# Optimization experiments

Hardware: AMD Instinct MI355X
Metric: run time of the kernel (lower is better)

## Reference

```python
import jax, jax.numpy as jnp
import numpy as np

B, C, H, W = 4, 64, 160, 160
OUT = 64
KS = (5, 7)


def conv2d(x, w, b=None, pad=0, groups=1):
    y = jax.lax.conv_general_dilated(
        x, w, (1, 1), [(pad, pad), (pad, pad)],
        feature_group_count=groups,
        dimension_numbers=('NCHW', 'OIHW', 'NCHW'))
    return y if b is None else y + b[None, :, None, None]


def bn_eval(x, g, b, m, v, eps=1e-5):
    s = g / jnp.sqrt(v + eps)
    return x * s[None, :, None, None] + (b - m * s)[None, :, None, None]


def boundary_attn(x, w1, b1, w2, b2):
    Cc = x.shape[1]
    kx = jnp.array([[-1., 0., 1.], [-2., 0., 2.], [-1., 0., 1.]], jnp.float32)
    ky = jnp.array([[-1., -2., -1.], [0., 0., 0.], [1., 2., 1.]], jnp.float32)
    sobel = jnp.concatenate([jnp.tile(kx[None, None], (Cc, 1, 1, 1)),
                             jnp.tile(ky[None, None], (Cc, 1, 1, 1))], axis=0)  # [2C,1,3,3]
    # grouped conv (groups=C): same output-channel grouping semantics as torch
    edge = jnp.abs(conv2d(x, sobel, pad=1, groups=Cc))
    edge = (edge[:, :Cc] + edge[:, Cc:]).mean(axis=1, keepdims=True)
    a = jax.nn.relu(conv2d(x, w1, b1, pad=1))
    a = conv2d(a, w2, b2, pad=0)
    a = jax.nn.sigmoid(a + edge)
    return x * a + x


def icc(off, half_k):
    # iterative cumulative constraint over the (small, static) K channel axis
    K = off.shape[1]
    cs = [None] * K
    cs[half_k] = off[:, half_k]
    for i in range(1, half_k + 1):
        cs[half_k - i] = 0.5 * cs[half_k - i + 1] + 0.5 * off[:, half_k - i]
        cs[half_k + i] = 0.5 * cs[half_k + i - 1] + 0.5 * off[:, half_k + i]
    c = jnp.stack(cs, axis=1)
    w = jnp.ones((K, 1, 3, 3), jnp.float32) / 9.0
    return conv2d(c, w, pad=1, groups=K)


def tumor_center(x):
    _, _, Hx, Wx = x.shape
    fs = x.mean(axis=1)  # [B,H,W]
    hg = jnp.arange(Hx, dtype=x.dtype)[None, :, None]
    wg = jnp.arange(Wx, dtype=x.dtype)[None, None, :]
    tot = fs.sum(axis=(1, 2)) + 1e-6
    return (fs * hg).sum(axis=(1, 2)) / tot, (fs * wg).sum(axis=(1, 2)) / tot


def dyn1d(x, kw, kb, K, O):
    # Original Dynamic1DConv reshapes x to [B*H*W, C, 1, 1] and grid_samples a
    # [1,K] grid per pixel. With align_corners=True a 1x1 input maps every grid
    # coordinate to ix=iy=0, so sampled[n,c,k] == x[b,c,h,w] for all k; the
    # bmm with per-pixel kernels followed by sum over C therefore collapses to
    # (sum_c x) * (sum_k kernels) -- same math, no giant gather materialized.
    Bx, _, Hx, Wx = x.shape
    ker = conv2d(x, kw, kb, pad=0).reshape(Bx, O, K, Hx, Wx)
    return x.sum(axis=1, keepdims=True) * ker.sum(axis=2)


def reference(x, ba_w1, ba_b1, ba_w2, ba_b2,
              off_w1, off_b1, off_bn_g, off_bn_b, off_bn_m, off_bn_v,
              off_w2, off_b2,
              rk5_w, rk5_b, rk7_w, rk7_b,
              lk5_w, lk5_b, lk7_w, lk7_b,
              sf_w, sf_b, sf_bn_g, sf_bn_b, sf_bn_m, sf_bn_v,
              fc_w, fc_b):
    residual = x  # in_channels == out_channels -> nn.Identity
    xa = boundary_attn(x, ba_w1, ba_b1, ba_w2, ba_b2)
    # offset branch (faithful to original; mathematically dead because the
    # per-pixel grid_sample ignores its grid -- see dyn1d). BN in eval mode.
    raw = conv2d(xa, off_w1, off_b1, pad=1)
    raw = jax.nn.relu(bn_eval(raw, off_bn_g, off_bn_b, off_bn_m, off_bn_v))
    raw = conv2d(raw, off_w2, off_b2, pad=1)
    sumk, idx = sum(KS), 0
    _offs = []
    for k in KS:
        _offs.append(icc(jnp.tanh(raw[:, idx:idx + k]), k // 2))
        _offs.append(icc(jnp.tanh(raw[:, sumk + idx:sumk + idx + k]), k // 2))
        idx += k
    _hc, _wc = tumor_center(xa)  # also dead w.r.t. output
    O = OUT // 2 // len(KS)  # 16 channels per scale per flow type
    feats = [dyn1d(xa, rk5_w, rk5_b, 5, O), dyn1d(xa, rk7_w, rk7_b, 7, O),
             dyn1d(xa, lk5_w, lk5_b, 5, O), dyn1d(xa, lk7_w, lk7_b, 7, O)]
    fusion = jnp.concatenate(feats, axis=1)  # [B, OUT, H, W]
    y = jax.nn.relu(bn_eval(conv2d(fusion, sf_w, sf_b, pad=1),
                            sf_bn_g, sf_bn_b, sf_bn_m, sf_bn_v))
    y = conv2d(y, fc_w, fc_b, pad=0)
    return y + residual


def setup_inputs() -> dict:
    key = jax.random.key(0)
    keys = iter(jax.random.split(key, 40))
    def nrm(shape, s=0.05):
        return jax.random.normal(next(keys), shape, jnp.float32) * s
    d = {}
    d['x'] = nrm((B, C, H, W), 1.0)
    d['ba_w1'] = nrm((C // 2, C, 3, 3)); d['ba_b1'] = nrm((C // 2,))
    d['ba_w2'] = nrm((1, C // 2, 1, 1)); d['ba_b2'] = nrm((1,))
    d['off_w1'] = nrm((C // 2, C, 3, 3)); d['off_b1'] = nrm((C // 2,))
    d['off_bn_g'] = 1.0 + nrm((C // 2,)); d['off_bn_b'] = nrm((C // 2,))
    d['off_bn_m'] = nrm((C // 2,))
    d['off_bn_v'] = jax.random.uniform(next(keys), (C // 2,), jnp.float32, 0.5, 1.5)
    d['off_w2'] = nrm((2 * sum(KS), C // 2, 3, 3)); d['off_b2'] = nrm((2 * sum(KS),))
    O = OUT // 2 // len(KS)
    for name, k in (('rk5', 5), ('rk7', 7), ('lk5', 5), ('lk7', 7)):
        d[name + '_w'] = nrm((O * k, C, 1, 1)); d[name + '_b'] = nrm((O * k,))
    d['sf_w'] = nrm((OUT, OUT, 3, 3)); d['sf_b'] = nrm((OUT,))
    d['sf_bn_g'] = 1.0 + nrm((OUT,)); d['sf_bn_b'] = nrm((OUT,))
    d['sf_bn_m'] = nrm((OUT,))
    d['sf_bn_v'] = jax.random.uniform(next(keys), (OUT,), jnp.float32, 0.5, 1.5)
    d['fc_w'] = nrm((OUT, OUT, 1, 1)); d['fc_b'] = nrm((OUT,))
    return d
```

## Files before the change

### kernel.cpp

```cpp
#include <hip/hip_runtime.h>
#include <hip/hip_bf16.h>
#include <math.h>

#define BB 4
#define CC 64
#define HH 160
#define WW 160
#define HWs (HH*WW)
#define NPIX (BB*HWs)

using bf16 = __hip_bfloat16;
typedef __attribute__((ext_vector_type(8)))  short short8v;
typedef __attribute__((ext_vector_type(16))) float float16v;

__device__ __forceinline__ unsigned short f2bfu(float f){
    union { bf16 h; unsigned short u; } cv; cv.h = __float2bfloat16(f); return cv.u;
}
__device__ __forceinline__ float bfu2f(unsigned short u){
    union { float f; unsigned int i; } cv; cv.i = ((unsigned int)u)<<16; return cv.f;
}
__device__ __forceinline__ float16v fzero16(){
    float16v z;
    #pragma unroll
    for(int i=0;i<16;i++) z[i]=0.f;
    return z;
}

constexpr int B1X1 = 0;
constexpr int SFBo = 64;
constexpr int SFWf = 128;
constexpr int BAWf = 18560;
constexpr int FUWf = 27776;
constexpr int FCWf = 29824;
constexpr int WS_FLOATS = 31872;

__global__ void k_prep(const float* __restrict__ rk5w, const float* __restrict__ rk5b,
                       const float* __restrict__ rk7w, const float* __restrict__ rk7b,
                       const float* __restrict__ lk5w, const float* __restrict__ lk5b,
                       const float* __restrict__ lk7w, const float* __restrict__ lk7b,
                       const float* __restrict__ sfw,  const float* __restrict__ sfb,
                       const float* __restrict__ bng,  const float* __restrict__ bnb,
                       const float* __restrict__ bnm,  const float* __restrict__ bnv,
                       const float* __restrict__ baw1, const float* __restrict__ fcw,
                       float* __restrict__ ws)
{
    int tid = blockIdx.x*blockDim.x + threadIdx.x;
    int nt  = gridDim.x*blockDim.x;
    for(int o=tid;o<64;o+=nt){
        int grp=o>>4, oo=o&15; int K=(grp&1)?7:5;
        const float* bp = (grp==0)?rk5b:(grp==1)?rk7b:(grp==2)?lk5b:lk7b;
        float s=0.f; for(int k=0;k<K;k++) s += bp[oo*K+k];
        ws[B1X1+o]=s;
    }
    for(int oc=tid;oc<64;oc+=nt){
        float sc = bng[oc]*rsqrtf(bnv[oc]+1e-5f);
        ws[SFBo+oc] = sfb[oc]*sc + bnb[oc] - bnm[oc]*sc;
    }
    unsigned short* sfwf = (unsigned short*)(ws + SFWf);
    for(int idx=tid; idx<36864; idx+=nt){
        int og = idx/18432;  int rem = idx - og*18432;
        int f  = rem>>9;     int r2 = rem & 511;
        int lane = r2>>3;    int j = r2&7;
        int tap = f>>2, kc = f&3;
        int oc = og*32 + (lane&31);
        int ic = kc*16 + (lane>>5)*8 + j;
        float sc = bng[oc]*rsqrtf(bnv[oc]+1e-5f);
        sfwf[idx] = f2bfu(sfw[(oc*64+ic)*9 + tap] * sc);
    }
    unsigned short* bawf = (unsigned short*)(ws + BAWf);
    for(int idx=tid; idx<18432; idx+=nt){
        int f  = idx>>9;     int r2 = idx & 511;
        int lane = r2>>3;    int j = r2&7;
        int tap = f>>2, kc = f&3;
        int oc = lane&31;
        int ic = kc*16 + (lane>>5)*8 + j;
        bawf[idx] = f2bfu(baw1[(oc*64+ic)*9 + tap]);
    }
    unsigned short* fuwf = (unsigned short*)(ws + FUWf);
    for(int idx=tid; idx<4096; idx+=nt){
        int og   = idx>>11;
        int kc   = (idx>>9)&3;
        int lane = (idx>>3)&63;
        int j    = idx&7;
        int oc = og*32 + (lane&31);
        int c  = kc*16 + (lane>>5)*8 + j;
        int grp = oc>>4, oo = oc&15; int K = (grp&1)?7:5;
        const float* w = (grp==0)?rk5w:(grp==1)?rk7w:(grp==2)?lk5w:lk7w;
        float s = 0.f;
        for(int k=0;k<K;k++) s += w[(oo*K+k)*64 + c];
        fuwf[idx] = f2bfu(s);
    }
    unsigned short* fcwf = (unsigned short*)(ws + FCWf);
    for(int idx=tid; idx<4096; idx+=nt){
        int og   = idx>>11;
        int kc   = (idx>>9)&3;
        int lane = (idx>>3)&63;
        int j    = idx&7;
        int oc = og*32 + (lane&31);
        int c  = kc*16 + (lane>>5)*8 + j;
        fcwf[idx] = f2bfu(fcw[oc*64 + c]);
    }
}

__global__ __launch_bounds__(256)
void k_x2nhwc(const float* __restrict__ x, unsigned short* __restrict__ xb)
{
    __shared__ unsigned short ls[128*72];
    const int t = threadIdx.x;
    const int p0 = blockIdx.x*128;
    const int b = p0 / HWs, pp0 = p0 % HWs;
    const float* xbase = x + (size_t)b*CC*HWs + pp0;
    #pragma unroll
    for(int iter=0; iter<32; iter++){
        int idx = iter*256 + t;
        int c = idx>>7, px = idx&127;
        int bs = (c>>3) ^ ((px>>3)&7);
        ls[px*72 + bs*8 + (c&7)] = f2bfu(xbase[(size_t)c*HWs + px]);
    }
    __syncthreads();
    #pragma unroll
    for(int iter=0; iter<4; iter++){
        int idx = iter*256 + t;
        int sub = idx&7, px = idx>>3;
        int bs = sub ^ ((px>>3)&7);
        short8v v = *(short8v*)(ls + px*72 + bs*8);
        *(short8v*)(xb + ((size_t)(p0+px))*64 + sub*8) = v;
    }
}

__global__ __launch_bounds__(256)
void k_fuseA(const unsigned short* __restrict__ xb, const float* __restrict__ bab1,
             const float* __restrict__ baw2, const float* __restrict__ bab2,
             const float* __restrict__ ws, unsigned short* __restrict__ fus)
{
    __shared__ unsigned short tile[10*18*72];
    __shared__ float zbuf[8][16];
    __shared__ float ebuf[2][128];
    __shared__ float sxbuf[8][16];
    __shared__ float pbuf[128], qbuf[128];
    const int bw = blockIdx.x, bh = blockIdx.y, b = blockIdx.z;
    const int t = threadIdx.x;
    const int wave = t>>6, lane = t&63;
    const int half = lane>>5, n = lane&31;
    const int w0 = bw*16, h0 = bh*8;

    const unsigned short* fb = xb + (size_t)b*HWs*64;
    for(int idx=t; idx<1440; idx+=256){
        int sub = idx&7; int pix = idx>>3;
        int row = pix/18, col = pix%18;
        int gh = h0-1+row, gw = w0-1+col;
        short8v v = {0,0,0,0,0,0,0,0};
        if(gh>=0&&gh<HH&&gw>=0&&gw<WW)
            v = *(const short8v*)(fb + ((size_t)(gh*WW+gw))*64 + sub*8);
        *(short8v*)(tile + (row*18+col)*72 + sub*8) = v;
    }
    float b1v[16], w2v[16];
    #pragma unroll
    for(int r=0;r<16;r++){
        int oc = (r&3) + 8*(r>>2) + 4*half;
        b1v[r] = bab1[oc];
        w2v[r] = baw2[oc];
    }
    __syncthreads();

    const unsigned short* bawf = (const unsigned short*)(ws + BAWf);
    {
        const int rbase = 2*wave + (n>>4);
        const int cbase = n&15;
        float16v acc = fzero16();
        #pragma unroll
        for(int kc=0; kc<4; kc++){
            short8v af[9];
            #pragma unroll
            for(int tap=0; tap<9; tap++)
                af[tap] = *(const short8v*)(bawf + (((size_t)(tap*4+kc))*64 + lane)*8);
            #pragma unroll
            for(int tap=0; tap<9; tap++){
                const int dh = tap/3, dw = tap%3;
                short8v bf = *(const short8v*)(tile + ((rbase+dh)*18 + cbase+dw)*72
                                               + kc*16 + half*8);
                acc = __builtin_amdgcn_mfma_f32_32x32x16_bf16(af[tap], bf, acc, 0,0,0);
            }
        }
        float cz = 0.f;
        #pragma unroll
        for(int r=0;r<16;r++) cz += fmaxf(acc[r]+b1v[r],0.f)*w2v[r];
        cz += __shfl_xor(cz, 32);
        if(lane < 32) zbuf[2*wave + (n>>4)][n&15] = cz;
    }
    {
        short8v ones;
        #pragma unroll
        for(int j=0;j<8;j++) ones[j] = (short)0x3F80;
        float16v s = fzero16();
        const int rr = 2*wave + (n>>4) + 1, cc = (n&15) + 1;
        #pragma unroll
        for(int kc=0; kc<4; kc++){
            short8v bf = *(const short8v*)(tile + (rr*18 + cc)*72 + kc*16 + half*8);
            s = __builtin_amdgcn_mfma_f32_32x32x16_bf16(ones, bf, s, 0,0,0);
        }
        if(lane < 32) sxbuf[2*wave + (n>>4)][n&15] = s[0];
    }
    {
        const int hf = t>>7, px = t&127;
        const int r = px>>4, c = px&15;
        float e = 0.f;
        #pragma unroll
        for(int s=0; s<4; s++){
            const int sub = hf*4 + s;
            if(hf==0){
                short8v a0 = *(const short8v*)(tile + ((r  )*18 + c  )*72 + sub*8);
                short8v a2 = *(const short8v*)(tile + ((r  )*18 + c+2)*72 + sub*8);
                short8v a3 = *(const short8v*)(tile + ((r+1)*18 + c  )*72 + sub*8);
                short8v a5 = *(const short8v*)(tile + ((r+1)*18 + c+2)*72 + sub*8);
                short8v a6 = *(const short8v*)(tile + ((r+2)*18 + c  )*72 + sub*8);
                short8v a8 = *(const short8v*)(tile + ((r+2)*18 + c+2)*72 + sub*8);
                #pragma unroll
                for(int j=0;j<8;j++){
                    float gx = (bfu2f((unsigned short)a2[j]) - bfu2f((unsigned short)a0[j]))
                       + 2.f*(bfu2f((unsigned short)a5[j]) - bfu2f((unsigned short)a3[j]))
                       +      (bfu2f((unsigned short)a8[j]) - bfu2f((unsigned short)a6[j]));
                    e += fabsf(gx);
                }
            } else {
                short8v b0 = *(const short8v*)(tile + ((r  )*18 + c  )*72 + sub*8);
                short8v b1 = *(const short8v*)(tile + ((r  )*18 + c+1)*72 + sub*8);
                short8v b2 = *(const short8v*)(tile + ((r  )*18 + c+2)*72 + sub*8);
                short8v b6 = *(const short8v*)(tile + ((r+2)*18 + c  )*72 + sub*8);
                short8v b7 = *(const short8v*)(tile + ((r+2)*18 + c+1)*72 + sub*8);
                short8v b8 = *(const short8v*)(tile + ((r+2)*18 + c+2)*72 + sub*8);
                #pragma unroll
                for(int j=0;j<8;j++){
                    float gy = (bfu2f((unsigned short)b6[j]) - bfu2f((unsigned short)b0[j]))
                       + 2.f*(bfu2f((unsigned short)b7[j]) - bfu2f((unsigned short)b1[j]))
                       +      (bfu2f((unsigned short)b8[j]) - bfu2f((unsigned short)b2[j]));
                    e += fabsf(gy);
                }
            }
        }
        ebuf[hf][px] = e;
    }
    __syncthreads();

    if(t < 128){
        const int row = t>>4, col = t&15;
        float z = zbuf[row][col] + bab2[0]
                + (ebuf[0][t] + ebuf[1][t]) * (1.f/32.f);
        float A = 1.f + 1.f/(1.f+__expf(-z));
        float S = A * sxbuf[row][col];
        pbuf[t] = A*S;
        qbuf[t] = S;
    }
    __syncthreads();

    {
        const int og = wave&1;
        const unsigned short* fuwf = (const unsigned short*)(ws + FUWf);
        short8v wf[4];
        #pragma unroll
        for(int kc=0; kc<4; kc++)
            wf[kc] = *(const short8v*)(fuwf + (((size_t)og*4 + kc)*64 + lane)*8);
        float bqv[16];
        #pragma unroll
        for(int r=0;r<16;r++) bqv[r] = ws[B1X1 + og*32 + (r&3)+8*(r>>2)+4*half];
        #pragma unroll
        for(int t2=0; t2<2; t2++){
            const int rp = (wave>>1) + 2*t2;
            const int row = 2*rp + (n>>4), col = n&15;
            float16v a = fzero16();
            #pragma unroll
            for(int kc=0; kc<4; kc++){
                short8v bf = *(const short8v*)(tile + ((row+1)*18 + col+1)*72
                                               + kc*16 + half*8);
                a = __builtin_amdgcn_mfma_f32_32x32x16_bf16(wf[kc], bf, a, 0,0,0);
            }
            const float P = pbuf[row*16+col], Q = qbuf[row*16+col];
            unsigned short* base = fus + ((size_t)b*HWs + (h0+row)*WW + w0+col)*64
                                   + og*32 + 4*half;
            #pragma unroll
            for(int g=0; g<4; g++){
                union { unsigned long long u; unsigned short s[4]; } pk;
                #pragma unroll
                for(int rr=0; rr<4; rr++)
                    pk.s[rr] = f2bfu(P*a[4*g+rr] + Q*bqv[4*g+rr]);
                *(unsigned long long*)(base + 8*g) = pk.u;
            }
        }
    }
}

__global__ __launch_bounds__(256)
void k_fuseB(const unsigned short* __restrict__ fus, const float* __restrict__ ws,
             const float* __restrict__ fcb, const float* __restrict__ x,
             float* __restrict__ out)
{
    __shared__ unsigned short ftile[10*18*72];
    __shared__ unsigned short ytile[128*72];
    const int bw = blockIdx.x, bh = blockIdx.y, b = blockIdx.z;
    const int t  = threadIdx.x;
    const int wave = t>>6, lane = t&63;
    const int half = lane>>5, n = lane&31;
    const int og = wave&1;
    const int w0 = bw*16, h0 = bh*8;

    const unsigned short* fb = fus + (size_t)b*HWs*64;
    for(int idx=t; idx<1440; idx+=256){
        int sub = idx&7; int pix = idx>>3;
        int row = pix/18, col = pix%18;
        int gh = h0-1+row, gw = w0-1+col;
        short8v v = {0,0,0,0,0,0,0,0};
        if(gh>=0&&gh<HH&&gw>=0&&gw<WW)
            v = *(const short8v*)(fb + ((size_t)(gh*WW+gw))*64 + sub*8);
        *(short8v*)(ftile + (row*18+col)*72 + sub*8) = v;
    }
    float biasv[16];
    #pragma unroll
    for(int r=0;r<16;r++) biasv[r] = ws[SFBo + og*32 + (r&3)+8*(r>>2)+4*half];
    __syncthreads();

    const unsigned short* sfwf = (const unsigned short*)(ws + SFWf);
    const int rp0 = wave>>1, rp1 = rp0+2;
    const int row0 = 2*rp0 + (n>>4), row1 = 2*rp1 + (n>>4), col = n&15;
    {
        float16v A0 = fzero16(), A1 = fzero16();
        #pragma unroll
        for(int kc=0; kc<4; kc++){
            short8v af[9];
            #pragma unroll
            for(int tap=0; tap<9; tap++)
                af[tap] = *(const short8v*)(sfwf + (((size_t)og*36 + tap*4+kc)*64 + lane)*8);
            #pragma unroll
            for(int tap=0; tap<9; tap++){
                const int dh = tap/3, dw = tap%3;
                short8v b0 = *(const short8v*)(ftile + ((row0+dh)*18 + col+dw)*72
                                               + kc*16 + half*8);
                short8v b1 = *(const short8v*)(ftile + ((row1+dh)*18 + col+dw)*72
                                               + kc*16 + half*8);
                A0 = __builtin_amdgcn_mfma_f32_32x32x16_bf16(af[tap], b0, A0, 0,0,0);
                A1 = __builtin_amdgcn_mfma_f32_32x32x16_bf16(af[tap], b1, A1, 0,0,0);
            }
        }
        unsigned short* y0 = ytile + (row0*16+col)*72 + og*32 + 4*half;
        unsigned short* y1p = ytile + (row1*16+col)*72 + og*32 + 4*half;
        #pragma unroll
        for(int g=0; g<4; g++){
            union { unsigned long long u; unsigned short s[4]; } pk0, pk1;
            #pragma unroll
            for(int rr=0; rr<4; rr++){
                pk0.s[rr] = f2bfu(fmaxf(A0[4*g+rr] + biasv[4*g+rr], 0.f));
                pk1.s[rr] = f2bfu(fmaxf(A1[4*g+rr] + biasv[4*g+rr], 0.f));
            }
            *(unsigned long long*)(y0  + 8*g) = pk0.u;
            *(unsigned long long*)(y1p + 8*g) = pk1.u;
        }
    }
    __syncthreads();

    {
        const unsigned short* fcwf = (const unsigned short*)(ws + FCWf);
        short8v ff[4];
        #pragma unroll
        for(int kc=0; kc<4; kc++)
            ff[kc] = *(const short8v*)(fcwf + (((size_t)og*4 + kc)*64 + lane)*8);
        float fcbv[16];
        #pragma unroll
        for(int r=0;r<16;r++) fcbv[r] = fcb[og*32 + (r&3)+8*(r>>2)+4*half];
        #pragma unroll
        for(int t2=0; t2<2; t2++){
            const int rp = (wave>>1) + 2*t2;
            const int row = 2*rp + (n>>4);
            const int px = row*16 + col;
            float16v F = fzero16();
            #pragma unroll
            for(int kc=0; kc<4; kc++){
                short8v bf = *(const short8v*)(ytile + px*72 + kc*16 + half*8);
                F = __builtin_amdgcn_mfma_f32_32x32x16_bf16(ff[kc], bf, F, 0,0,0);
            }
            #pragma unroll
            for(int r=0;r<16;r++){
                int oc = og*32 + (r&3)+8*(r>>2)+4*half;
                size_t g = ((size_t)(b*CC + oc))*HWs + (h0+row)*WW + w0 + col;
                out[g] = F[r] + fcbv[r] + x[g];
            }
        }
    }
}

extern "C" void kernel_launch(void* const* d_in, const int* in_sizes, int n_in,
                              void* d_out, int out_size, void* d_ws, size_t ws_size,
                              hipStream_t stream)
{
    const float* x     = (const float*)d_in[0];
    const float* ba_w1 = (const float*)d_in[1];
    const float* ba_b1 = (const float*)d_in[2];
    const float* ba_w2 = (const float*)d_in[3];
    const float* ba_b2 = (const float*)d_in[4];
    const float* rk5_w = (const float*)d_in[13];
    const float* rk5_b = (const float*)d_in[14];
    const float* rk7_w = (const float*)d_in[15];
    const float* rk7_b = (const float*)d_in[16];
    const float* lk5_w = (const float*)d_in[17];
    const float* lk5_b = (const float*)d_in[18];
    const float* lk7_w = (const float*)d_in[19];
    const float* lk7_b = (const float*)d_in[20];
    const float* sf_w  = (const float*)d_in[21];
    const float* sf_b  = (const float*)d_in[22];
    const float* bng   = (const float*)d_in[23];
    const float* bnb   = (const float*)d_in[24];
    const float* bnm   = (const float*)d_in[25];
    const float* bnv   = (const float*)d_in[26];
    const float* fc_w  = (const float*)d_in[27];
    const float* fc_b  = (const float*)d_in[28];

    float* wsf = (float*)d_ws;
    unsigned short* XB  = (unsigned short*)((char*)d_ws + (size_t)WS_FLOATS*4);
    unsigned short* FUS = XB + (size_t)NPIX*64;
    float* out = (float*)d_out;

    k_prep<<<64, 256, 0, stream>>>(rk5_w,rk5_b,rk7_w,rk7_b,lk5_w,lk5_b,lk7_w,lk7_b,
                                   sf_w,sf_b,bng,bnb,bnm,bnv, ba_w1, fc_w, wsf);
    k_x2nhwc<<<NPIX/128, 256, 0, stream>>>(x, XB);
    k_fuseA<<<dim3(10,20,4), 256, 0, stream>>>(XB, ba_b1, ba_w2, ba_b2, wsf, FUS);
    k_fuseB<<<dim3(10,20,4), 256, 0, stream>>>(FUS, wsf, fc_b, x, out);
}
```

Measured before the change: 184.9 us.

## Keep per-pixel intermediates in registers and chain conv-to-1x1 via lane shuffles

The NCHW-to-NHWC transpose kernel now reads x with float4 loads instead of scalar loads. In fuseA, each wave keeps its own pixel's attention scalars in registers and computes both output-channel halves itself. This removes the zbuf/sxbuf/pbuf/qbuf shared staging and one barrier. In the final kernel, each wave computes all 64 channels of the 3x3 conv for its rows and feeds the bf16 result straight into the 1x1 MFMA through cross-half lane shuffles, which removes the ytile shared buffer and a barrier. The cost is more registers per wave, fewer independent MFMA chains per wave, and redundant weight loads.

```diff
diff --git a/kernel.cpp b/kernel.cpp
--- a/kernel.cpp
+++ b/kernel.cpp
@@ -109,13 +109,19 @@
     const int t = threadIdx.x;
     const int p0 = blockIdx.x*128;
     const int b = p0 / HWs, pp0 = p0 % HWs;
-    const float* xbase = x + (size_t)b*CC*HWs + pp0;
-    #pragma unroll
-    for(int iter=0; iter<32; iter++){
+    const float4* xb4 = (const float4*)(x + (size_t)b*CC*HWs + pp0);
+    #pragma unroll
+    for(int iter=0; iter<8; iter++){
         int idx = iter*256 + t;
-        int c = idx>>7, px = idx&127;
-        int bs = (c>>3) ^ ((px>>3)&7);
-        ls[px*72 + bs*8 + (c&7)] = f2bfu(xbase[(size_t)c*HWs + px]);
+        int c = idx>>5, g = idx&31;
+        float4 v = xb4[(size_t)c*(HWs/4) + g];
+        int px = g*4;
+        int bs = (c>>3) ^ ((g>>1)&7);
+        unsigned short* base = ls + bs*8 + (c&7);
+        base[(px+0)*72] = f2bfu(v.x);
+        base[(px+1)*72] = f2bfu(v.y);
+        base[(px+2)*72] = f2bfu(v.z);
+        base[(px+3)*72] = f2bfu(v.w);
     }
     __syncthreads();
     #pragma unroll
@@ -134,10 +140,7 @@
              const float* __restrict__ ws, unsigned short* __restrict__ fus)
 {
     __shared__ unsigned short tile[10*18*72];
-    __shared__ float zbuf[8][16];
     __shared__ float ebuf[2][128];
-    __shared__ float sxbuf[8][16];
-    __shared__ float pbuf[128], qbuf[128];
     const int bw = blockIdx.x, bh = blockIdx.y, b = blockIdx.z;
     const int t = threadIdx.x;
     const int wave = t>>6, lane = t&63;
@@ -163,10 +166,11 @@
     }
     __syncthreads();
 
-    const unsigned short* bawf = (const unsigned short*)(ws + BAWf);
+    const int row = 2*wave + (n>>4), col = n&15;
+
+    float cz;
     {
-        const int rbase = 2*wave + (n>>4);
-        const int cbase = n&15;
+        const unsigned short* bawf = (const unsigned short*)(ws + BAWf);
         float16v acc = fzero16();
         #pragma unroll
         for(int kc=0; kc<4; kc++){
@@ -177,29 +181,28 @@
             #pragma unroll
             for(int tap=0; tap<9; tap++){
                 const int dh = tap/3, dw = tap%3;
-                short8v bf = *(const short8v*)(tile + ((rbase+dh)*18 + cbase+dw)*72
+                short8v bf = *(const short8v*)(tile + ((row+dh)*18 + col+dw)*72
                                                + kc*16 + half*8);
                 acc = __builtin_amdgcn_mfma_f32_32x32x16_bf16(af[tap], bf, acc, 0,0,0);
             }
         }
-        float cz = 0.f;
+        cz = 0.f;
         #pragma unroll
         for(int r=0;r<16;r++) cz += fmaxf(acc[r]+b1v[r],0.f)*w2v[r];
         cz += __shfl_xor(cz, 32);
-        if(lane < 32) zbuf[2*wave + (n>>4)][n&15] = cz;
-    }
+    }
+    float sx;
     {
         short8v ones;
         #pragma unroll
         for(int j=0;j<8;j++) ones[j] = (short)0x3F80;
         float16v s = fzero16();
-        const int rr = 2*wave + (n>>4) + 1, cc = (n&15) + 1;
         #pragma unroll
         for(int kc=0; kc<4; kc++){
-            short8v bf = *(const short8v*)(tile + (rr*18 + cc)*72 + kc*16 + half*8);
+            short8v bf = *(const short8v*)(tile + ((row+1)*18 + col+1)*72 + kc*16 + half*8);
             s = __builtin_amdgcn_mfma_f32_32x32x16_bf16(ones, bf, s, 0,0,0);
         }
-        if(lane < 32) sxbuf[2*wave + (n>>4)][n&15] = s[0];
+        sx = s[0];
     }
     {
         const int hf = t>>7, px = t&127;
@@ -242,49 +245,34 @@
     }
     __syncthreads();
 
-    if(t < 128){
-        const int row = t>>4, col = t&15;
-        float z = zbuf[row][col] + bab2[0]
-                + (ebuf[0][t] + ebuf[1][t]) * (1.f/32.f);
-        float A = 1.f + 1.f/(1.f+__expf(-z));
-        float S = A * sxbuf[row][col];
-        pbuf[t] = A*S;
-        qbuf[t] = S;
-    }
-    __syncthreads();
-
-    {
-        const int og = wave&1;
-        const unsigned short* fuwf = (const unsigned short*)(ws + FUWf);
-        short8v wf[4];
-        #pragma unroll
-        for(int kc=0; kc<4; kc++)
-            wf[kc] = *(const short8v*)(fuwf + (((size_t)og*4 + kc)*64 + lane)*8);
-        float bqv[16];
-        #pragma unroll
-        for(int r=0;r<16;r++) bqv[r] = ws[B1X1 + og*32 + (r&3)+8*(r>>2)+4*half];
-        #pragma unroll
-        for(int t2=0; t2<2; t2++){
-            const int rp = (wave>>1) + 2*t2;
-            const int row = 2*rp + (n>>4), col = n&15;
-            float16v a = fzero16();
+    const int pxl = row*16 + col;
+    float z = cz + bab2[0] + (ebuf[0][pxl] + ebuf[1][pxl]) * (1.f/32.f);
+    float A = 1.f + 1.f/(1.f+__expf(-z));
+    float Q = A * sx;
+    float P = A * Q;
+
+    const unsigned short* fuwf = (const unsigned short*)(ws + FUWf);
+    #pragma unroll
+    for(int og=0; og<2; og++){
+        float16v a = fzero16();
+        #pragma unroll
+        for(int kc=0; kc<4; kc++){
+            short8v wf = *(const short8v*)(fuwf + (((size_t)og*4 + kc)*64 + lane)*8);
+            short8v bf = *(const short8v*)(tile + ((row+1)*18 + col+1)*72 + kc*16 + half*8);
+            a = __builtin_amdgcn_mfma_f32_32x32x16_bf16(wf, bf, a, 0,0,0);
+        }
+        float bq[16];
+        #pragma unroll
+        for(int r=0;r<16;r++) bq[r] = ws[B1X1 + og*32 + (r&3)+8*(r>>2)+4*half];
+        unsigned short* base = fus + ((size_t)b*HWs + (h0+row)*WW + w0+col)*64
+                               + og*32 + 4*half;
+        #pragma unroll
+        for(int g=0; g<4; g++){
+            union { unsigned long long u; unsigned short s[4]; } pk;
             #pragma unroll
-            for(int kc=0; kc<4; kc++){
-                short8v bf = *(const short8v*)(tile + ((row+1)*18 + col+1)*72
-                                               + kc*16 + half*8);
-                a = __builtin_amdgcn_mfma_f32_32x32x16_bf16(wf[kc], bf, a, 0,0,0);
-            }
-            const float P = pbuf[row*16+col], Q = qbuf[row*16+col];
-            unsigned short* base = fus + ((size_t)b*HWs + (h0+row)*WW + w0+col)*64
-                                   + og*32 + 4*half;
-            #pragma unroll
-            for(int g=0; g<4; g++){
-                union { unsigned long long u; unsigned short s[4]; } pk;
-                #pragma unroll
-                for(int rr=0; rr<4; rr++)
-                    pk.s[rr] = f2bfu(P*a[4*g+rr] + Q*bqv[4*g+rr]);
-                *(unsigned long long*)(base + 8*g) = pk.u;
-            }
+            for(int rr=0; rr<4; rr++)
+                pk.s[rr] = f2bfu(P*a[4*g+rr] + Q*bq[4*g+rr]);
+            *(unsigned long long*)(base + 8*g) = pk.u;
         }
     }
 }
@@ -295,12 +283,10 @@
              float* __restrict__ out)
 {
     __shared__ unsigned short ftile[10*18*72];
-    __shared__ unsigned short ytile[128*72];
     const int bw = blockIdx.x, bh = blockIdx.y, b = blockIdx.z;
     const int t  = threadIdx.x;
     const int wave = t>>6, lane = t&63;
     const int half = lane>>5, n = lane&31;
-    const int og = wave&1;
     const int w0 = bw*16, h0 = bh*8;
 
     const unsigned short* fb = fus + (size_t)b*HWs*64;
@@ -313,16 +299,16 @@
             v = *(const short8v*)(fb + ((size_t)(gh*WW+gw))*64 + sub*8);
         *(short8v*)(ftile + (row*18+col)*72 + sub*8) = v;
     }
-    float biasv[16];
-    #pragma unroll
-    for(int r=0;r<16;r++) biasv[r] = ws[SFBo + og*32 + (r&3)+8*(r>>2)+4*half];
     __syncthreads();
 
+    const int row = 2*wave + (n>>4), col = n&15;
     const unsigned short* sfwf = (const unsigned short*)(ws + SFWf);
-    const int rp0 = wave>>1, rp1 = rp0+2;
-    const int row0 = 2*rp0 + (n>>4), row1 = 2*rp1 + (n>>4), col = n&15;
-    {
-        float16v A0 = fzero16(), A1 = fzero16();
+    const unsigned short* fcwf = (const unsigned short*)(ws + FCWf);
+    float16v F0 = fzero16(), F1 = fzero16();
+
+    #pragma unroll
+    for(int og=0; og<2; og++){
+        float16v Y = fzero16();
         #pragma unroll
         for(int kc=0; kc<4; kc++){
             short8v af[9];
@@ -332,56 +318,52 @@
             #pragma unroll
             for(int tap=0; tap<9; tap++){
                 const int dh = tap/3, dw = tap%3;
-                short8v b0 = *(const short8v*)(ftile + ((row0+dh)*18 + col+dw)*72
+                short8v bf = *(const short8v*)(ftile + ((row+dh)*18 + col+dw)*72
                                                + kc*16 + half*8);
-                short8v b1 = *(const short8v*)(ftile + ((row1+dh)*18 + col+dw)*72
-                                               + kc*16 + half*8);
-                A0 = __builtin_amdgcn_mfma_f32_32x32x16_bf16(af[tap], b0, A0, 0,0,0);
-                A1 = __builtin_amdgcn_mfma_f32_32x32x16_bf16(af[tap], b1, A1, 0,0,0);
+                Y = __builtin_amdgcn_mfma_f32_32x32x16_bf16(af[tap], bf, Y, 0,0,0);
             }
         }
-        unsigned short* y0 = ytile + (row0*16+col)*72 + og*32 + 4*half;
-        unsigned short* y1p = ytile + (row1*16+col)*72 + og*32 + 4*half;
-        #pragma unroll
-        for(int g=0; g<4; g++){
-            union { unsigned long long u; unsigned short s[4]; } pk0, pk1;
-            #pragma unroll
-            for(int rr=0; rr<4; rr++){
-                pk0.s[rr] = f2bfu(fmaxf(A0[4*g+rr] + biasv[4*g+rr], 0.f));
-                pk1.s[rr] = f2bfu(fmaxf(A1[4*g+rr] + biasv[4*g+rr], 0.f));
-            }
-            *(unsigned long long*)(y0  + 8*g) = pk0.u;
-            *(unsigned long long*)(y1p + 8*g) = pk1.u;
-        }
-    }
-    __syncthreads();
-
-    {
-        const unsigned short* fcwf = (const unsigned short*)(ws + FCWf);
-        short8v ff[4];
-        #pragma unroll
-        for(int kc=0; kc<4; kc++)
-            ff[kc] = *(const short8v*)(fcwf + (((size_t)og*4 + kc)*64 + lane)*8);
-        float fcbv[16];
-        #pragma unroll
-        for(int r=0;r<16;r++) fcbv[r] = fcb[og*32 + (r&3)+8*(r>>2)+4*half];
-        #pragma unroll
-        for(int t2=0; t2<2; t2++){
-            const int rp = (wave>>1) + 2*t2;
-            const int row = 2*rp + (n>>4);
-            const int px = row*16 + col;
-            float16v F = fzero16();
-            #pragma unroll
-            for(int kc=0; kc<4; kc++){
-                short8v bf = *(const short8v*)(ytile + px*72 + kc*16 + half*8);
-                F = __builtin_amdgcn_mfma_f32_32x32x16_bf16(ff[kc], bf, F, 0,0,0);
-            }
-            #pragma unroll
-            for(int r=0;r<16;r++){
-                int oc = og*32 + (r&3)+8*(r>>2)+4*half;
-                size_t g = ((size_t)(b*CC + oc))*HWs + (h0+row)*WW + w0 + col;
-                out[g] = F[r] + fcbv[r] + x[g];
-            }
+        unsigned short yb[16];
+        #pragma unroll
+        for(int r=0;r<16;r++){
+            float bias = ws[SFBo + og*32 + (r&3)+8*(r>>2)+4*half];
+            yb[r] = f2bfu(fmaxf(Y[r] + bias, 0.f));
+        }
+        #pragma unroll
+        for(int kcl=0; kcl<2; kcl++){
+            const int kc_fc = 2*og + kcl;
+            unsigned short l0,l1,l2,l3, s0,s1,s2,s3;
+            if(half==0){ l0=yb[8*kcl+0]; l1=yb[8*kcl+1]; l2=yb[8*kcl+2]; l3=yb[8*kcl+3];
+                         s0=yb[8*kcl+4]; s1=yb[8*kcl+5]; s2=yb[8*kcl+6]; s3=yb[8*kcl+7]; }
+            else       { l0=yb[8*kcl+4]; l1=yb[8*kcl+5]; l2=yb[8*kcl+6]; l3=yb[8*kcl+7];
+                         s0=yb[8*kcl+0]; s1=yb[8*kcl+1]; s2=yb[8*kcl+2]; s3=yb[8*kcl+3]; }
+            int p0 = (int)((unsigned)s0 | ((unsigned)s1<<16));
+            int p1 = (int)((unsigned)s2 | ((unsigned)s3<<16));
+            int r0 = __shfl_xor(p0, 32);
+            int r1 = __shfl_xor(p1, 32);
+            unsigned short m0 = (unsigned short)(r0 & 0xffff);
+            unsigned short m1 = (unsigned short)(((unsigned)r0) >> 16);
+            unsigned short m2 = (unsigned short)(r1 & 0xffff);
+            unsigned short m3 = (unsigned short)(((unsigned)r1) >> 16);
+            short8v B;
+            if(half==0){ B[0]=(short)l0; B[1]=(short)l1; B[2]=(short)l2; B[3]=(short)l3;
+                         B[4]=(short)m0; B[5]=(short)m1; B[6]=(short)m2; B[7]=(short)m3; }
+            else       { B[0]=(short)m0; B[1]=(short)m1; B[2]=(short)m2; B[3]=(short)m3;
+                         B[4]=(short)l0; B[5]=(short)l1; B[6]=(short)l2; B[7]=(short)l3; }
+            short8v fa0 = *(const short8v*)(fcwf + (((size_t)0*4 + kc_fc)*64 + lane)*8);
+            short8v fa1 = *(const short8v*)(fcwf + (((size_t)1*4 + kc_fc)*64 + lane)*8);
+            F0 = __builtin_amdgcn_mfma_f32_32x32x16_bf16(fa0, B, F0, 0,0,0);
+            F1 = __builtin_amdgcn_mfma_f32_32x32x16_bf16(fa1, B, F1, 0,0,0);
+        }
+    }
+    #pragma unroll
+    for(int og=0; og<2; og++){
+        #pragma unroll
+        for(int r=0;r<16;r++){
+            int oc = og*32 + (r&3)+8*(r>>2)+4*half;
+            size_t g = ((size_t)(b*CC + oc))*HWs + (h0+row)*WW + w0 + col;
+            float v = (og==0) ? F0[r] : F1[r];
+            out[g] = v + fcb[oc] + x[g];
         }
     }
 }
```

Measured after the change: 176.8 us. -4.4%, faster.
